# Kernel tuning notes

Measured on AMD Instinct MI355X. Metric: run time of the kernel, lower is better.

## Reference

```python
import jax, jax.numpy as jnp
import numpy as np

D = 1024
H = 16
HD = D // H
S = 2048
B = 2
HID = D * 7 // 2  # 3584


def _linear_params(key, din, dout):
    kw, kb = jax.random.split(key)
    bound = 1.0 / np.sqrt(din)
    W = jax.random.uniform(kw, (dout, din), jnp.float32, -bound, bound)
    b = jax.random.uniform(kb, (dout,), jnp.float32, -bound, bound)
    return W, b


def setup_inputs() -> dict:
    key = jax.random.key(0)
    ks = jax.random.split(key, 9)
    x = jax.random.normal(ks[0], (B, S, D), jnp.float32)
    pos_emb = 0.02 * jax.random.normal(ks[1], (1, S, D), jnp.float32)
    q_w, q_b = _linear_params(ks[2], D, D)
    k_w, k_b = _linear_params(ks[3], D, D)
    v_w, v_b = _linear_params(ks[4], D, D)
    o_w, o_b = _linear_params(ks[5], D, D)
    in_w, in_b = _linear_params(ks[6], D, HID)
    gate_w, gate_b = _linear_params(ks[7], D, HID)
    out_w, out_b = _linear_params(ks[8], HID, D)
    norm1_w = jnp.ones((D,), jnp.float32)
    norm2_w = jnp.ones((D,), jnp.float32)
    return dict(x=x, pos_emb=pos_emb, norm1_w=norm1_w, norm2_w=norm2_w,
                q_w=q_w, q_b=q_b, k_w=k_w, k_b=k_b, v_w=v_w, v_b=v_b,
                o_w=o_w, o_b=o_b, in_w=in_w, in_b=in_b,
                gate_w=gate_w, gate_b=gate_b, out_w=out_w, out_b=out_b)


def _rmsnorm(x, w, eps=1e-6):
    return x * jax.lax.rsqrt(jnp.mean(x * x, axis=-1, keepdims=True) + eps) * w


def _attn(x, q_w, q_b, k_w, k_b, v_w, v_b, o_w, o_b):
    b, s, _ = x.shape
    q = (x @ q_w.T + q_b).reshape(b, s, H, HD)
    k = (x @ k_w.T + k_b).reshape(b, s, H, HD)
    v = (x @ v_w.T + v_b).reshape(b, s, H, HD)
    scores = jnp.einsum('bqhd,bkhd->bhqk', q, k) / jnp.sqrt(jnp.float32(HD))
    causal = jnp.tril(jnp.ones((s, s), bool))  # True = keep
    scores = jnp.where(causal, scores, -jnp.inf)
    p = jax.nn.softmax(scores, axis=-1)
    o = jnp.einsum('bhqk,bkhd->bqhd', p, v).reshape(b, s, D)
    return o @ o_w.T + o_b


def _mlp(x, in_w, in_b, gate_w, gate_b, out_w, out_b):
    gate = jax.nn.silu(x @ gate_w.T + gate_b)
    h = gate * (x @ in_w.T + in_b)
    return h @ out_w.T + out_b


def reference(x, pos_emb, norm1_w, norm2_w, q_w, q_b, k_w, k_b, v_w, v_b,
              o_w, o_b, in_w, in_b, gate_w, gate_b, out_w, out_b):
    x = x + pos_emb
    x = x + _attn(_rmsnorm(x, norm1_w), q_w, q_b, k_w, k_b, v_w, v_b, o_w, o_b)
    x = x + _mlp(_rmsnorm(x, norm2_w), in_w, in_b, gate_w, gate_b, out_w, out_b)
    return x
```

## Files before the change

kernel.cpp:

```cpp
#include <hip/hip_runtime.h>

typedef __attribute__((ext_vector_type(4))) float f32x4;
typedef __attribute__((ext_vector_type(8))) short bf16x8;
typedef unsigned short u16;

constexpr int kB = 2, kS = 2048, kD = 1024, kH = 16, kHD = 64, kHID = 3584;
constexpr int kN = kB * kS;

__device__ __forceinline__ u16 f2bf(float f) {
  unsigned u = __float_as_uint(f);
  u = (u + 0x7FFFu + ((u >> 16) & 1u)) >> 16;
  return (u16)u;
}
__device__ __forceinline__ float bf2f(u16 v) {
  return __uint_as_float((unsigned)v << 16);
}

#define AS1(p) ((const __attribute__((address_space(1))) void*)(p))
#define AS3(p) ((__attribute__((address_space(3))) void*)(p))

__global__ __launch_bounds__(256) void k_prep(
    const float* __restrict__ x, const float* __restrict__ pos,
    const float* __restrict__ w, float* __restrict__ xr, u16* __restrict__ xn) {
  const int n = blockIdx.x, t = threadIdx.x, s = n & (kS - 1);
  float4 a = ((const float4*)(x + (size_t)n * kD))[t];
  float4 p = ((const float4*)(pos + (size_t)s * kD))[t];
  a.x += p.x; a.y += p.y; a.z += p.z; a.w += p.w;
  ((float4*)(xr + (size_t)n * kD))[t] = a;
  float ss = a.x*a.x + a.y*a.y + a.z*a.z + a.w*a.w;
#pragma unroll
  for (int off = 1; off < 64; off <<= 1) ss += __shfl_xor(ss, off);
  __shared__ float red[4];
  if ((t & 63) == 0) red[t >> 6] = ss;
  __syncthreads();
  float rs = rsqrtf((red[0] + red[1] + red[2] + red[3]) * (1.0f / kD) + 1e-6f);
  float4 wv = ((const float4*)w)[t];
  ushort4 o;
  o.x = f2bf(a.x * rs * wv.x); o.y = f2bf(a.y * rs * wv.y);
  o.z = f2bf(a.z * rs * wv.z); o.w = f2bf(a.w * rs * wv.w);
  ((ushort4*)(xn + (size_t)n * kD))[t] = o;
}

__global__ __launch_bounds__(256) void k_rms2(
    const float* __restrict__ xin, const float* __restrict__ w, u16* __restrict__ xn) {
  const int n = blockIdx.x, t = threadIdx.x;
  float4 a = ((const float4*)(xin + (size_t)n * kD))[t];
  float ss = a.x*a.x + a.y*a.y + a.z*a.z + a.w*a.w;
#pragma unroll
  for (int off = 1; off < 64; off <<= 1) ss += __shfl_xor(ss, off);
  __shared__ float red[4];
  if ((t & 63) == 0) red[t >> 6] = ss;
  __syncthreads();
  float rs = rsqrtf((red[0] + red[1] + red[2] + red[3]) * (1.0f / kD) + 1e-6f);
  float4 wv = ((const float4*)w)[t];
  ushort4 o;
  o.x = f2bf(a.x * rs * wv.x); o.y = f2bf(a.y * rs * wv.y);
  o.z = f2bf(a.z * rs * wv.z); o.w = f2bf(a.w * rs * wv.w);
  ((ushort4*)(xn + (size_t)n * kD))[t] = o;
}

__device__ __forceinline__ void cvt4(const float* __restrict__ s, u16* __restrict__ d, int j) {
  float4 v = ((const float4*)s)[j];
  ushort4 o;
  o.x = f2bf(v.x); o.y = f2bf(v.y); o.z = f2bf(v.z); o.w = f2bf(v.w);
  ((ushort4*)d)[j] = o;
}

__global__ __launch_bounds__(256) void k_wprep(
    const float* __restrict__ q_w, const float* __restrict__ k_w,
    const float* __restrict__ v_w, const float* __restrict__ o_w,
    const float* __restrict__ in_w, const float* __restrict__ gate_w,
    const float* __restrict__ out_w,
    const float* __restrict__ q_b, const float* __restrict__ k_b,
    const float* __restrict__ v_b,
    u16* __restrict__ W, float* __restrict__ bqkv) {
  const int i = blockIdx.x * 256 + threadIdx.x;
  if (i < 262144)       cvt4(q_w,    W + 0,        i);
  else if (i < 524288)  cvt4(k_w,    W + 1048576,  i - 262144);
  else if (i < 786432)  cvt4(v_w,    W + 2097152,  i - 524288);
  else if (i < 1048576) cvt4(o_w,    W + 3145728,  i - 786432);
  else if (i < 1966080) cvt4(in_w,   W + 4194304,  i - 1048576);
  else if (i < 2883584) cvt4(gate_w, W + 7864320,  i - 1966080);
  else if (i < 3801088) cvt4(out_w,  W + 11534336, i - 2883584);
  else {
    const int j = i - 3801088;
    const float* src = j < 256 ? q_b : (j < 512 ? k_b : v_b);
    ((float4*)bqkv)[j] = ((const float4*)src)[j & 255];
  }
}

template <int MODE, int BM>
__global__ __launch_bounds__(256) void k_gemm(
    const u16* __restrict__ A, const u16* __restrict__ Bw,
    const float* __restrict__ bias, const void* extra,
    void* outp, int M, int N, int K) {
  constexpr int ASEG = BM / 16;
  constexpr int NSEG = ASEG + 8;
  constexpr int WROWS = BM / 2;
  constexpr int MF = BM / 32;
  __shared__ __align__(16) u16 As[BM * 32];
  __shared__ __align__(16) u16 Bs[128 * 32];
  const int tid = threadIdx.x, lane = tid & 63, wv_ = tid >> 6;
  const int lr = lane & 15, lg = lane >> 4;
  const int brow = blockIdx.y * BM, bcol = blockIdx.x * 128;
  const int wr = wv_ >> 1, wc = wv_ & 1;

  const f32x4 zz = {0.f, 0.f, 0.f, 0.f};
  f32x4 acc[MF][4];
#pragma unroll
  for (int m = 0; m < MF; m++)
#pragma unroll
    for (int n = 0; n < 4; n++) acc[m][n] = zz;

  for (int kt = 0; kt < K; kt += 32) {
#pragma unroll
    for (int i = 0; i < NSEG / 4; ++i) {
      const int seg = i * 4 + wv_;
      const int rsub = (seg < ASEG) ? seg : seg - ASEG;
      const int row = rsub * 16 + (lane >> 2), cs = lane & 3;
      if (seg < ASEG) {
        __builtin_amdgcn_global_load_lds(AS1(A + (size_t)(brow + row) * K + kt + cs * 8),
                                         AS3((char*)As + (size_t)seg * 1024), 16, 0, 0);
      } else {
        __builtin_amdgcn_global_load_lds(AS1(Bw + (size_t)(bcol + row) * K + kt + cs * 8),
                                         AS3((char*)Bs + (size_t)(seg - ASEG) * 1024), 16, 0, 0);
      }
    }
    __syncthreads();
    bf16x8 af[MF], bfr[4];
#pragma unroll
    for (int m = 0; m < MF; m++) af[m] = *(const bf16x8*)&As[(wr * WROWS + m * 16 + lr) * 32 + lg * 8];
#pragma unroll
    for (int n = 0; n < 4; n++) bfr[n] = *(const bf16x8*)&Bs[(wc * 64 + n * 16 + lr) * 32 + lg * 8];
#pragma unroll
    for (int m = 0; m < MF; m++)
#pragma unroll
      for (int n = 0; n < 4; n++)
        acc[m][n] = __builtin_amdgcn_mfma_f32_16x16x32_bf16(af[m], bfr[n], acc[m][n], 0, 0, 0);
    __syncthreads();
  }

#pragma unroll
  for (int m = 0; m < MF; m++) {
    const int row0 = brow + wr * WROWS + m * 16 + lg * 4;
#pragma unroll
    for (int n = 0; n < 4; n++) {
      const int col = bcol + wc * 64 + n * 16 + lr;
      const float bv = bias[col];
#pragma unroll
      for (int r = 0; r < 4; r++) {
        const size_t idx = (size_t)(row0 + r) * N + col;
        float v = acc[m][n][r] + bv;
        if (MODE == 0) {
          ((u16*)outp)[idx] = f2bf(v);
        } else if (MODE == 1) {
          ((float*)outp)[idx] = v + ((const float*)extra)[idx];
        } else {
          float g = v / (1.0f + __expf(-v));
          ((u16*)outp)[idx] = f2bf(g * bf2f(((const u16*)extra)[idx]));
        }
      }
    }
  }
}

__global__ __launch_bounds__(256) void k_attn(
    const u16* __restrict__ qkv, u16* __restrict__ attn_o) {
  __shared__ __align__(16) u16 Ks[64 * 64];
  __shared__ __align__(16) u16 Vt[64 * 64];
  __shared__ __align__(16) u16 Pl[4][16 * 64];

  const int tid = threadIdx.x, lane = tid & 63, w = tid >> 6;
  const int lr = lane & 15, lg = lane >> 4;
  const int p = blockIdx.x, bh = blockIdx.y;
  const int b = bh >> 4, h = bh & 15;
  const int qbL = p, qbH = 31 - p;
  const size_t base = (size_t)b * kS;
  const f32x4 zz = {0.f, 0.f, 0.f, 0.f};

  bf16x8 qfL[2], qfH[2];
#pragma unroll
  for (int ks = 0; ks < 2; ks++) {
    qfL[ks] = *(const bf16x8*)&qkv[(base + qbL * 64 + w * 16 + lr) * 3072 + h * 64 + ks * 32 + lg * 8];
    qfH[ks] = *(const bf16x8*)&qkv[(base + qbH * 64 + w * 16 + lr) * 3072 + h * 64 + ks * 32 + lg * 8];
  }

  f32x4 oL[4], oH[4];
  float mL[4], lLr[4], mH[4], lHr[4];
#pragma unroll
  for (int nb = 0; nb < 4; nb++) { oL[nb] = zz; oH[nb] = zz; }
#pragma unroll
  for (int r = 0; r < 4; r++) { mL[r] = -1e30f; mH[r] = -1e30f; lLr[r] = 0.f; lHr[r] = 0.f; }

  const int srow = tid >> 2, scol = (tid & 3) * 16;
  int4 kr0, kr1, vr0, vr1;
  auto issue = [&](int t) {
    const size_t rowb = (base + t * 64 + srow) * 3072 + h * 64;
    kr0 = *(const int4*)&qkv[rowb + 1024 + scol];
    kr1 = *(const int4*)&qkv[rowb + 1024 + scol + 8];
    vr0 = *(const int4*)&qkv[rowb + 2048 + scol];
    vr1 = *(const int4*)&qkv[rowb + 2048 + scol + 8];
  };
  auto commit = [&]() {
    const int bo0 = (srow * 128 + scol * 2) ^ ((srow & 7) << 4);
    const int bo1 = (srow * 128 + scol * 2 + 16) ^ ((srow & 7) << 4);
    *(int4*)((char*)Ks + bo0) = kr0;
    *(int4*)((char*)Ks + bo1) = kr1;
    const u16* ve0 = (const u16*)&vr0;
    const u16* ve1 = (const u16*)&vr1;
#pragma unroll
    for (int j = 0; j < 8; j++) {
      const int d0 = scol + j;
      *(u16*)((char*)Vt + ((d0 * 128 + srow * 2) ^ ((d0 & 7) << 4))) = ve0[j];
      const int d1 = scol + 8 + j;
      *(u16*)((char*)Vt + ((d1 * 128 + srow * 2) ^ ((d1 & 7) << 4))) = ve1[j];
    }
  };

  auto compute = [&](const bf16x8* qf, f32x4* oacc, float* mrow, float* lrow,
                     int qb, int t, bool masked) {
    f32x4 sc[4];
#pragma unroll
    for (int hn = 0; hn < 4; hn++) sc[hn] = zz;
#pragma unroll
    for (int hn = 0; hn < 4; hn++) {
      const int krow = hn * 16 + lr;
#pragma unroll
      for (int ks = 0; ks < 2; ks++) {
        const int bo = (krow * 128 + (ks * 32 + lg * 8) * 2) ^ ((krow & 7) << 4);
        bf16x8 kf = *(const bf16x8*)((const char*)Ks + bo);
        sc[hn] = __builtin_amdgcn_mfma_f32_16x16x32_bf16(qf[ks], kf, sc[hn], 0, 0, 0);
      }
    }
    float alpha[4];
#pragma unroll
    for (int r = 0; r < 4; r++) {
      const int qa = qb * 64 + w * 16 + lg * 4 + r;
      float s0 = sc[0][r] * 0.125f, s1 = sc[1][r] * 0.125f;
      float s2 = sc[2][r] * 0.125f, s3 = sc[3][r] * 0.125f;
      if (masked) {
        if (t * 64 + lr > qa) s0 = -1e30f;
        if (t * 64 + 16 + lr > qa) s1 = -1e30f;
        if (t * 64 + 32 + lr > qa) s2 = -1e30f;
        if (t * 64 + 48 + lr > qa) s3 = -1e30f;
      }
      float mx = fmaxf(fmaxf(s0, s1), fmaxf(s2, s3));
#pragma unroll
      for (int off = 1; off < 16; off <<= 1) mx = fmaxf(mx, __shfl_xor(mx, off));
      const float mnew = fmaxf(mrow[r], mx);
      alpha[r] = __expf(mrow[r] - mnew);
      mrow[r] = mnew;
      s0 = __expf(s0 - mnew); s1 = __expf(s1 - mnew);
      s2 = __expf(s2 - mnew); s3 = __expf(s3 - mnew);
      sc[0][r] = s0; sc[1][r] = s1; sc[2][r] = s2; sc[3][r] = s3;
      float ps = (s0 + s1) + (s2 + s3);
#pragma unroll
      for (int off = 1; off < 16; off <<= 1) ps += __shfl_xor(ps, off);
      lrow[r] = lrow[r] * alpha[r] + ps;
    }
#pragma unroll
    for (int nb = 0; nb < 4; nb++)
#pragma unroll
      for (int r = 0; r < 4; r++) oacc[nb][r] *= alpha[r];
    char* pw = (char*)&Pl[w][0];
#pragma unroll
    for (int hn = 0; hn < 4; hn++)
#pragma unroll
      for (int r = 0; r < 4; r++) {
        const int prow = lg * 4 + r, pcol = hn * 16 + lr;
        *(u16*)(pw + ((prow * 128 + pcol * 2) ^ ((prow & 7) << 4))) = f2bf(sc[hn][r]);
      }
    bf16x8 pf[2];
#pragma unroll
    for (int ks = 0; ks < 2; ks++)
      pf[ks] = *(const bf16x8*)((const char*)pw + ((lr * 128 + (ks * 32 + lg * 8) * 2) ^ ((lr & 7) << 4)));
#pragma unroll
    for (int nb = 0; nb < 4; nb++) {
      const int vrow = nb * 16 + lr;
#pragma unroll
      for (int ks = 0; ks < 2; ks++) {
        const int bo = (vrow * 128 + (ks * 32 + lg * 8) * 2) ^ ((vrow & 7) << 4);
        bf16x8 vf = *(const bf16x8*)((const char*)Vt + bo);
        oacc[nb] = __builtin_amdgcn_mfma_f32_16x16x32_bf16(pf[ks], vf, oacc[nb], 0, 0, 0);
      }
    }
  };

  const int ntS = qbH + 1;
  issue(0);
  commit();
  __syncthreads();
  for (int t = 0; t < ntS; ++t) {
    const bool haveNext = (t + 1 < ntS);
    if (haveNext) issue(t + 1);
    compute(qfH, oH, mH, lHr, qbH, t, t == qbH);
    if (t <= qbL) compute(qfL, oL, mL, lLr, qbL, t, t == qbL);
    __syncthreads();
    if (haveNext) commit();
    __syncthreads();
  }

  auto epi = [&](f32x4* oacc, float* lrow, int qb) {
#pragma unroll
    for (int nb = 0; nb < 4; nb++)
#pragma unroll
      for (int r = 0; r < 4; r++) {
        const int q = qb * 64 + w * 16 + lg * 4 + r;
        attn_o[(base + q) * kD + h * 64 + nb * 16 + lr] = f2bf(oacc[nb][r] / lrow[r]);
      }
  };
  epi(oH, lHr, qbH);
  epi(oL, lLr, qbL);
}

constexpr size_t OFF_XR   = 0;
constexpr size_t OFF_XN1  = OFF_XR  + (size_t)kN * kD * 4;
constexpr size_t OFF_XN2  = OFF_XN1 + (size_t)kN * kD * 2;
constexpr size_t OFF_W    = OFF_XN2 + (size_t)kN * kD * 2;
constexpr size_t OFF_BQKV = OFF_W + 15204352ull * 2;
constexpr size_t OFF_ACT  = OFF_BQKV + 3072 * 4;

extern "C" void kernel_launch(void* const* d_in, const int* in_sizes, int n_in,
                              void* d_out, int out_size, void* d_ws, size_t ws_size,
                              hipStream_t stream) {
  const float* x     = (const float*)d_in[0];
  const float* pos   = (const float*)d_in[1];
  const float* n1w   = (const float*)d_in[2];
  const float* n2w   = (const float*)d_in[3];
  const float* q_w   = (const float*)d_in[4];
  const float* q_b   = (const float*)d_in[5];
  const float* k_w   = (const float*)d_in[6];
  const float* k_b   = (const float*)d_in[7];
  const float* v_w   = (const float*)d_in[8];
  const float* v_b   = (const float*)d_in[9];
  const float* o_w   = (const float*)d_in[10];
  const float* o_b   = (const float*)d_in[11];
  const float* in_w  = (const float*)d_in[12];
  const float* in_b  = (const float*)d_in[13];
  const float* gate_w= (const float*)d_in[14];
  const float* gate_b= (const float*)d_in[15];
  const float* out_w = (const float*)d_in[16];
  const float* out_b = (const float*)d_in[17];
  float* outf = (float*)d_out;
  char* ws = (char*)d_ws;

  float* xr   = (float*)(ws + OFF_XR);
  u16*   xn1  = (u16*)(ws + OFF_XN1);
  u16*   xn2  = (u16*)(ws + OFF_XN2);
  u16*   W    = (u16*)(ws + OFF_W);
  float* bqkv = (float*)(ws + OFF_BQKV);
  u16*   qkv  = (u16*)(ws + OFF_ACT);
  u16*   attn_o = (u16*)(ws + OFF_ACT + (size_t)kN * 3072 * 2);
  u16*   inoutb = (u16*)(ws + OFF_ACT);
  u16*   hb     = (u16*)(ws + OFF_ACT + (size_t)kN * kHID * 2);

  u16* Wq   = W + 0;
  u16* Wo   = W + 3145728;
  u16* Win  = W + 4194304;
  u16* Wg   = W + 7864320;
  u16* Wout = W + 11534336;

  k_prep<<<kN, 256, 0, stream>>>(x, pos, n1w, xr, xn1);
  k_wprep<<<14851, 256, 0, stream>>>(q_w, k_w, v_w, o_w, in_w, gate_w, out_w,
                                     q_b, k_b, v_b, W, bqkv);

  k_gemm<0, 128><<<dim3(24, 32), 256, 0, stream>>>(xn1, Wq, bqkv, nullptr, qkv, kN, 3072, kD);

  k_attn<<<dim3(16, kB * kH), 256, 0, stream>>>(qkv, attn_o);

  k_gemm<1, 64><<<dim3(8, 64), 256, 0, stream>>>(attn_o, Wo, o_b, xr, outf, kN, kD, kD);

  k_rms2<<<kN, 256, 0, stream>>>(outf, n2w, xn2);

  k_gemm<0, 128><<<dim3(28, 32), 256, 0, stream>>>(xn2, Win, in_b, nullptr, inoutb, kN, kHID, kD);
  k_gemm<3, 128><<<dim3(28, 32), 256, 0, stream>>>(xn2, Wg, gate_b, inoutb, hb, kN, kHID, kD);

  k_gemm<1, 64><<<dim3(8, 64), 256, 0, stream>>>(hb, Wout, out_b, outf, outf, kN, kD, kHID);
}
```

Baseline: 507.3 us.

## Double-buffer attention K/V, use DPP row max and MFMA row sums, remap GEMM blocks per XCD

The attention kernel now double-buffers K/V in shared memory, which removes one barrier per tile. The row max uses DPP row shifts instead of shuffles. The row-sum reduction is replaced by an extra MFMA of P against a vector of ones. GEMM launches become 1D grids whose block ids are remapped so that consecutive tiles land on the same XCD (chunked by 8), aiming for better L2 reuse. The cost is twice the attention LDS and extra MFMA work for the sums, and the row sums are now accumulated from the bf16-rounded P.

```diff
diff --git a/kernel.cpp b/kernel.cpp
--- a/kernel.cpp
+++ b/kernel.cpp
@@ -14,6 +14,19 @@
 }
 __device__ __forceinline__ float bf2f(u16 v) {
   return __uint_as_float((unsigned)v << 16);
+}
+
+__device__ __forceinline__ float rowmax16(float v) {
+  int t;
+  t = __builtin_amdgcn_update_dpp(0, __float_as_int(v), 0x121, 0xf, 0xf, true);
+  v = fmaxf(v, __int_as_float(t));
+  t = __builtin_amdgcn_update_dpp(0, __float_as_int(v), 0x122, 0xf, 0xf, true);
+  v = fmaxf(v, __int_as_float(t));
+  t = __builtin_amdgcn_update_dpp(0, __float_as_int(v), 0x124, 0xf, 0xf, true);
+  v = fmaxf(v, __int_as_float(t));
+  t = __builtin_amdgcn_update_dpp(0, __float_as_int(v), 0x128, 0xf, 0xf, true);
+  v = fmaxf(v, __int_as_float(t));
+  return v;
 }
 
 #define AS1(p) ((const __attribute__((address_space(1))) void*)(p))
@@ -93,7 +106,7 @@
 __global__ __launch_bounds__(256) void k_gemm(
     const u16* __restrict__ A, const u16* __restrict__ Bw,
     const float* __restrict__ bias, const void* extra,
-    void* outp, int M, int N, int K) {
+    void* outp, int M, int N, int K, int nbx) {
   constexpr int ASEG = BM / 16;
   constexpr int NSEG = ASEG + 8;
   constexpr int WROWS = BM / 2;
@@ -102,7 +115,9 @@
   __shared__ __align__(16) u16 Bs[128 * 32];
   const int tid = threadIdx.x, lane = tid & 63, wv_ = tid >> 6;
   const int lr = lane & 15, lg = lane >> 4;
-  const int brow = blockIdx.y * BM, bcol = blockIdx.x * 128;
+  const int chunk = gridDim.x >> 3;
+  const int sid = (blockIdx.x & 7) * chunk + (blockIdx.x >> 3);
+  const int brow = (sid / nbx) * BM, bcol = (sid % nbx) * 128;
   const int wr = wv_ >> 1, wc = wv_ & 1;
 
   const f32x4 zz = {0.f, 0.f, 0.f, 0.f};
@@ -166,8 +181,8 @@
 
 __global__ __launch_bounds__(256) void k_attn(
     const u16* __restrict__ qkv, u16* __restrict__ attn_o) {
-  __shared__ __align__(16) u16 Ks[64 * 64];
-  __shared__ __align__(16) u16 Vt[64 * 64];
+  __shared__ __align__(16) u16 Ks[2][64 * 64];
+  __shared__ __align__(16) u16 Vt[2][64 * 64];
   __shared__ __align__(16) u16 Pl[4][16 * 64];
 
   const int tid = threadIdx.x, lane = tid & 63, w = tid >> 6;
@@ -177,6 +192,9 @@
   const int qbL = p, qbH = 31 - p;
   const size_t base = (size_t)b * kS;
   const f32x4 zz = {0.f, 0.f, 0.f, 0.f};
+  bf16x8 vones;
+#pragma unroll
+  for (int j = 0; j < 8; j++) vones[j] = (short)0x3F80;
 
   bf16x8 qfL[2], qfH[2];
 #pragma unroll
@@ -185,12 +203,13 @@
     qfH[ks] = *(const bf16x8*)&qkv[(base + qbH * 64 + w * 16 + lr) * 3072 + h * 64 + ks * 32 + lg * 8];
   }
 
-  f32x4 oL[4], oH[4];
-  float mL[4], lLr[4], mH[4], lHr[4];
+  f32x4 oL[4], oH[4], lL, lH;
+  float mL[4], mH[4];
 #pragma unroll
   for (int nb = 0; nb < 4; nb++) { oL[nb] = zz; oH[nb] = zz; }
-#pragma unroll
-  for (int r = 0; r < 4; r++) { mL[r] = -1e30f; mH[r] = -1e30f; lLr[r] = 0.f; lHr[r] = 0.f; }
+  lL = zz; lH = zz;
+#pragma unroll
+  for (int r = 0; r < 4; r++) { mL[r] = -1e30f; mH[r] = -1e30f; }
 
   const int srow = tid >> 2, scol = (tid & 3) * 16;
   int4 kr0, kr1, vr0, vr1;
@@ -201,24 +220,28 @@
     vr0 = *(const int4*)&qkv[rowb + 2048 + scol];
     vr1 = *(const int4*)&qkv[rowb + 2048 + scol + 8];
   };
-  auto commit = [&]() {
+  auto commit = [&](int buf) {
+    char* kb = (char*)&Ks[buf][0];
+    char* vb = (char*)&Vt[buf][0];
     const int bo0 = (srow * 128 + scol * 2) ^ ((srow & 7) << 4);
     const int bo1 = (srow * 128 + scol * 2 + 16) ^ ((srow & 7) << 4);
-    *(int4*)((char*)Ks + bo0) = kr0;
-    *(int4*)((char*)Ks + bo1) = kr1;
+    *(int4*)(kb + bo0) = kr0;
+    *(int4*)(kb + bo1) = kr1;
     const u16* ve0 = (const u16*)&vr0;
     const u16* ve1 = (const u16*)&vr1;
 #pragma unroll
     for (int j = 0; j < 8; j++) {
       const int d0 = scol + j;
-      *(u16*)((char*)Vt + ((d0 * 128 + srow * 2) ^ ((d0 & 7) << 4))) = ve0[j];
+      *(u16*)(vb + ((d0 * 128 + srow * 2) ^ ((d0 & 7) << 4))) = ve0[j];
       const int d1 = scol + 8 + j;
-      *(u16*)((char*)Vt + ((d1 * 128 + srow * 2) ^ ((d1 & 7) << 4))) = ve1[j];
+      *(u16*)(vb + ((d1 * 128 + srow * 2) ^ ((d1 & 7) << 4))) = ve1[j];
     }
   };
 
-  auto compute = [&](const bf16x8* qf, f32x4* oacc, float* mrow, float* lrow,
-                     int qb, int t, bool masked) {
+  auto compute = [&](const bf16x8* qf, f32x4* oacc, f32x4& lacc, float* mrow,
+                     int qb, int t, bool masked, int buf) {
+    const char* kbuf = (const char*)&Ks[buf][0];
+    const char* vbuf = (const char*)&Vt[buf][0];
     f32x4 sc[4];
 #pragma unroll
     for (int hn = 0; hn < 4; hn++) sc[hn] = zz;
@@ -228,7 +251,7 @@
 #pragma unroll
       for (int ks = 0; ks < 2; ks++) {
         const int bo = (krow * 128 + (ks * 32 + lg * 8) * 2) ^ ((krow & 7) << 4);
-        bf16x8 kf = *(const bf16x8*)((const char*)Ks + bo);
+        bf16x8 kf = *(const bf16x8*)(kbuf + bo);
         sc[hn] = __builtin_amdgcn_mfma_f32_16x16x32_bf16(qf[ks], kf, sc[hn], 0, 0, 0);
       }
     }
@@ -244,24 +267,19 @@
         if (t * 64 + 32 + lr > qa) s2 = -1e30f;
         if (t * 64 + 48 + lr > qa) s3 = -1e30f;
       }
-      float mx = fmaxf(fmaxf(s0, s1), fmaxf(s2, s3));
-#pragma unroll
-      for (int off = 1; off < 16; off <<= 1) mx = fmaxf(mx, __shfl_xor(mx, off));
+      float mx = rowmax16(fmaxf(fmaxf(s0, s1), fmaxf(s2, s3)));
       const float mnew = fmaxf(mrow[r], mx);
       alpha[r] = __expf(mrow[r] - mnew);
       mrow[r] = mnew;
-      s0 = __expf(s0 - mnew); s1 = __expf(s1 - mnew);
-      s2 = __expf(s2 - mnew); s3 = __expf(s3 - mnew);
-      sc[0][r] = s0; sc[1][r] = s1; sc[2][r] = s2; sc[3][r] = s3;
-      float ps = (s0 + s1) + (s2 + s3);
-#pragma unroll
-      for (int off = 1; off < 16; off <<= 1) ps += __shfl_xor(ps, off);
-      lrow[r] = lrow[r] * alpha[r] + ps;
+      sc[0][r] = __expf(s0 - mnew); sc[1][r] = __expf(s1 - mnew);
+      sc[2][r] = __expf(s2 - mnew); sc[3][r] = __expf(s3 - mnew);
     }
 #pragma unroll
     for (int nb = 0; nb < 4; nb++)
 #pragma unroll
       for (int r = 0; r < 4; r++) oacc[nb][r] *= alpha[r];
+#pragma unroll
+    for (int r = 0; r < 4; r++) lacc[r] *= alpha[r];
     char* pw = (char*)&Pl[w][0];
 #pragma unroll
     for (int hn = 0; hn < 4; hn++)
@@ -280,37 +298,40 @@
 #pragma unroll
       for (int ks = 0; ks < 2; ks++) {
         const int bo = (vrow * 128 + (ks * 32 + lg * 8) * 2) ^ ((vrow & 7) << 4);
-        bf16x8 vf = *(const bf16x8*)((const char*)Vt + bo);
+        bf16x8 vf = *(const bf16x8*)(vbuf + bo);
         oacc[nb] = __builtin_amdgcn_mfma_f32_16x16x32_bf16(pf[ks], vf, oacc[nb], 0, 0, 0);
       }
     }
+#pragma unroll
+    for (int ks = 0; ks < 2; ks++)
+      lacc = __builtin_amdgcn_mfma_f32_16x16x32_bf16(pf[ks], vones, lacc, 0, 0, 0);
   };
 
   const int ntS = qbH + 1;
   issue(0);
-  commit();
+  commit(0);
   __syncthreads();
   for (int t = 0; t < ntS; ++t) {
     const bool haveNext = (t + 1 < ntS);
+    const int buf = t & 1;
     if (haveNext) issue(t + 1);
-    compute(qfH, oH, mH, lHr, qbH, t, t == qbH);
-    if (t <= qbL) compute(qfL, oL, mL, lLr, qbL, t, t == qbL);
-    __syncthreads();
-    if (haveNext) commit();
+    compute(qfH, oH, lH, mH, qbH, t, t == qbH, buf);
+    if (t <= qbL) compute(qfL, oL, lL, mL, qbL, t, t == qbL, buf);
+    if (haveNext) commit(buf ^ 1);
     __syncthreads();
   }
 
-  auto epi = [&](f32x4* oacc, float* lrow, int qb) {
+  auto epi = [&](f32x4* oacc, f32x4& lacc, int qb) {
 #pragma unroll
     for (int nb = 0; nb < 4; nb++)
 #pragma unroll
       for (int r = 0; r < 4; r++) {
         const int q = qb * 64 + w * 16 + lg * 4 + r;
-        attn_o[(base + q) * kD + h * 64 + nb * 16 + lr] = f2bf(oacc[nb][r] / lrow[r]);
+        attn_o[(base + q) * kD + h * 64 + nb * 16 + lr] = f2bf(oacc[nb][r] / lacc[r]);
       }
   };
-  epi(oH, lHr, qbH);
-  epi(oL, lLr, qbL);
+  epi(oH, lH, qbH);
+  epi(oL, lL, qbL);
 }
 
 constexpr size_t OFF_XR   = 0;
@@ -364,16 +385,16 @@
   k_wprep<<<14851, 256, 0, stream>>>(q_w, k_w, v_w, o_w, in_w, gate_w, out_w,
                                      q_b, k_b, v_b, W, bqkv);
 
-  k_gemm<0, 128><<<dim3(24, 32), 256, 0, stream>>>(xn1, Wq, bqkv, nullptr, qkv, kN, 3072, kD);
+  k_gemm<0, 128><<<768, 256, 0, stream>>>(xn1, Wq, bqkv, nullptr, qkv, kN, 3072, kD, 24);
 
   k_attn<<<dim3(16, kB * kH), 256, 0, stream>>>(qkv, attn_o);
 
-  k_gemm<1, 64><<<dim3(8, 64), 256, 0, stream>>>(attn_o, Wo, o_b, xr, outf, kN, kD, kD);
+  k_gemm<1, 64><<<512, 256, 0, stream>>>(attn_o, Wo, o_b, xr, outf, kN, kD, kD, 8);
 
   k_rms2<<<kN, 256, 0, stream>>>(outf, n2w, xn2);
 
-  k_gemm<0, 128><<<dim3(28, 32), 256, 0, stream>>>(xn2, Win, in_b, nullptr, inoutb, kN, kHID, kD);
-  k_gemm<3, 128><<<dim3(28, 32), 256, 0, stream>>>(xn2, Wg, gate_b, inoutb, hb, kN, kHID, kD);
-
-  k_gemm<1, 64><<<dim3(8, 64), 256, 0, stream>>>(hb, Wout, out_b, outf, outf, kN, kD, kHID);
-}
+  k_gemm<0, 128><<<896, 256, 0, stream>>>(xn2, Win, in_b, nullptr, inoutb, kN, kHID, kD, 28);
+  k_gemm<3, 128><<<896, 256, 0, stream>>>(xn2, Wg, gate_b, inoutb, hb, kN, kHID, kD, 28);
+
+  k_gemm<1, 64><<<512, 256, 0, stream>>>(hb, Wout, out_b, outf, outf, kN, kD, kHID, 8);
+}
```

Result: slower. 525.8 us (+3.6%).
